# Kernel optimization log

Hardware: AMD Instinct MI355X
Metric: run time of the kernel (lower is better)

## Reference

```python
import jax, jax.numpy as jnp
import numpy as np

L, H, NH, NKV, HD, S, P, FF = 2, 2048, 16, 2, 128, 1024, 1024, 5632
G = NH // NKV
THETA = 1000000.0
EPS = 1e-6
SCALE = 1.0 / np.sqrt(HD).astype(np.float32)


def rms_norm(x, w):
    return x * jax.lax.rsqrt(jnp.mean(x * x, axis=-1, keepdims=True) + EPS) * w


def rotate_half(x):
    x1, x2 = jnp.split(x, 2, axis=-1)
    return jnp.concatenate([-x2, x1], axis=-1)


def setup_inputs() -> dict:
    key = jax.random.key(0)
    ks = iter(jax.random.split(key, 16))
    w = lambda shape: jax.random.normal(next(ks), shape, jnp.float32) * 0.02
    return {
        'inputs_embeds': jax.random.normal(next(ks), (1, S, H), jnp.float32),
        'position_ids': (jnp.arange(S, dtype=jnp.int32) + P)[None, :],
        'past_k': jax.random.normal(next(ks), (L, 1, NKV, P, HD), jnp.float32),
        'past_v': jax.random.normal(next(ks), (L, 1, NKV, P, HD), jnp.float32),
        'ln1_w': jnp.ones((L, H), jnp.float32),
        'wq': w((L, H, NH * HD)), 'bq': jnp.zeros((L, NH * HD), jnp.float32),
        'wk': w((L, H, NKV * HD)), 'bk': jnp.zeros((L, NKV * HD), jnp.float32),
        'wv': w((L, H, NKV * HD)), 'bv': jnp.zeros((L, NKV * HD), jnp.float32),
        'wo': w((L, NH * HD, H)),
        'ln2_w': jnp.ones((L, H), jnp.float32),
        'w_gate': w((L, H, FF)), 'w_up': w((L, H, FF)), 'w_down': w((L, FF, H)),
        'norm_w': jnp.ones((H,), jnp.float32),
    }


def reference(inputs_embeds, position_ids, past_k, past_v, ln1_w, wq, bq, wk, bk,
              wv, bv, wo, ln2_w, w_gate, w_up, w_down, norm_w):
    pos = position_ids.astype(jnp.float32)                      # [1,S]
    inv_freq = 1.0 / (THETA ** (jnp.arange(0, HD, 2, dtype=jnp.float32) / HD))
    freqs = pos[:, :, None] * inv_freq                          # [1,S,HD/2]
    emb = jnp.concatenate([freqs, freqs], axis=-1)              # [1,S,HD]
    cos = jnp.cos(emb)[:, None]                                 # [1,1,S,HD]
    sin = jnp.sin(emb)[:, None]
    T = P + S
    k_pos = jnp.arange(T, dtype=jnp.float32)
    # causal mask over absolute positions: future keys masked with -65504
    mask = jnp.where(k_pos[None, None, None, :] > pos[:, None, :, None],
                     jnp.float32(-65504.0), jnp.float32(0.0))   # [1,1,S,T]

    hidden = inputs_embeds
    present = []
    for i in range(L):
        residual = hidden
        h = rms_norm(hidden, ln1_w[i])
        q = (h @ wq[i] + bq[i]).reshape(1, S, NH, HD).transpose(0, 2, 1, 3)
        k = (h @ wk[i] + bk[i]).reshape(1, S, NKV, HD).transpose(0, 2, 1, 3)
        v = (h @ wv[i] + bv[i]).reshape(1, S, NKV, HD).transpose(0, 2, 1, 3)
        q = q * cos + rotate_half(q) * sin
        k = k * cos + rotate_half(k) * sin
        k = jnp.concatenate([past_k[i], k], axis=2)             # [1,NKV,T,HD]
        v = jnp.concatenate([past_v[i], v], axis=2)
        present.append(k)
        present.append(v)
        # GQA: group query heads per kv head instead of expanding k/v
        qg = q.reshape(1, NKV, G, S, HD)
        attn = jnp.einsum('bkgsd,bktd->bkgst', qg, k) * SCALE   # [1,NKV,G,S,T]
        attn = jax.nn.softmax(attn + mask[:, :, None], axis=-1)
        out = jnp.einsum('bkgst,bktd->bkgsd', attn, v)
        out = out.reshape(1, NH, S, HD).transpose(0, 2, 1, 3).reshape(1, S, H)
        hidden = residual + out @ wo[i]
        residual = hidden
        h = rms_norm(hidden, ln2_w[i])
        h = (jax.nn.silu(h @ w_gate[i]) * (h @ w_up[i])) @ w_down[i]
        hidden = residual + h
    hidden = rms_norm(hidden, norm_w)
    return (hidden, *present)
```

## Files before the change

### kernel.cpp

```cpp
#include <hip/hip_runtime.h>

#define L_ 2
#define H_ 2048
#define NH_ 16
#define NKV_ 2
#define HD_ 128
#define S_ 1024
#define P_ 1024
#define T_ 2048
#define FF_ 5632
#define QKVN_ 2560
#define KOFF_ 2048
#define VOFF_ 2304

#define EPS_ 1e-6f
#define SCALE_ 0.08838834764831845f
#define DEFER_THR_ 8.0f

typedef __bf16 bf16_t;
typedef unsigned int u32;
typedef __bf16 bx8 __attribute__((ext_vector_type(8)));
typedef __bf16 bx4 __attribute__((ext_vector_type(4)));
typedef float  fx4 __attribute__((ext_vector_type(4)));

__device__ __forceinline__ fx4 mfma16(bx8 a, bx8 b, fx4 c) {
  return __builtin_amdgcn_mfma_f32_16x16x32_bf16(a, b, c, 0, 0, 0);
}

#define GLL16(gsrc, ldst) __builtin_amdgcn_global_load_lds( \
    (__attribute__((address_space(1))) void*)(gsrc),        \
    (__attribute__((address_space(3))) void*)(ldst), 16, 0, 0)

__device__ __forceinline__ bx8 lds_read_b128(char* p) {
  u32 a = (u32)(uintptr_t)(__attribute__((address_space(3))) void*)p;
  bx8 d;
  asm volatile("ds_read_b128 %0, %1" : "=v"(d) : "v"(a));
  return d;
}
__device__ __forceinline__ void lds_write_b16(char* p, float v) {
  u32 a = (u32)(uintptr_t)(__attribute__((address_space(3))) void*)p;
  bf16_t b = (bf16_t)v;
  u32 d = (u32)__builtin_bit_cast(unsigned short, b);
  asm volatile("ds_write_b16 %0, %1" :: "v"(a), "v"(d));
}

#define LGKM(n) asm volatile("s_waitcnt lgkmcnt(" #n ")" ::: "memory"); __builtin_amdgcn_sched_barrier(0)

__device__ __forceinline__ int xcd_swizzle(int orig, int nwg) {
  int q = nwg >> 3, r = nwg & 7;
  int xcd = orig & 7, lid = orig >> 3;
  return (xcd < r ? xcd * (q + 1) : r * (q + 1) + (xcd - r) * q) + lid;
}

__global__ void k_rope_tables(const int* __restrict__ pos, float* __restrict__ ct, float* __restrict__ st) {
  int i = blockIdx.x * 256 + threadIdx.x;
  if (i >= S_ * 64) return;
  int s = i >> 6, d = i & 63;
  float p = (float)pos[s];
  float inv = expf(-(float)(2 * d) * (13.815510557964274f / 128.0f));
  float f = p * inv;
  ct[i] = cosf(f);
  st[i] = sinf(f);
}

__global__ void k_copy4(const float* __restrict__ in, float* __restrict__ out, int n4) {
  int i = blockIdx.x * 256 + threadIdx.x;
  if (i < n4) ((fx4*)out)[i] = ((const fx4*)in)[i];
}

__global__ void k_cbias(const float* __restrict__ bq, const float* __restrict__ bk,
                        const float* __restrict__ bv, float* __restrict__ cb) {
  int i = blockIdx.x * 256 + threadIdx.x;
  if (i >= L_ * QKVN_) return;
  int l = i / QKVN_, j = i % QKVN_;
  float v;
  if (j < KOFF_)      v = bq[l * KOFF_ + j];
  else if (j < VOFF_) v = bk[l * (NKV_ * HD_) + j - KOFF_];
  else                v = bv[l * (NKV_ * HD_) + j - VOFF_];
  cb[i] = v;
}

template<int OUTBF>
__global__ __launch_bounds__(256) void k_rmsnorm(const float* __restrict__ x, const float* __restrict__ w,
                                                 void* __restrict__ y) {
  int row = blockIdx.x, tid = threadIdx.x;
  const fx4* xr = (const fx4*)(x + (size_t)row * H_);
  fx4 v0 = xr[tid], v1 = xr[tid + 256];
  float ss = v0[0]*v0[0] + v0[1]*v0[1] + v0[2]*v0[2] + v0[3]*v0[3]
           + v1[0]*v1[0] + v1[1]*v1[1] + v1[2]*v1[2] + v1[3]*v1[3];
  #pragma unroll
  for (int off = 32; off > 0; off >>= 1) ss += __shfl_xor(ss, off);
  __shared__ float red[4];
  if ((tid & 63) == 0) red[tid >> 6] = ss;
  __syncthreads();
  float tot = red[0] + red[1] + red[2] + red[3];
  float rs = rsqrtf(tot * (1.0f / H_) + EPS_);
  const fx4* wr_ = (const fx4*)w;
  fx4 w0 = wr_[tid], w1 = wr_[tid + 256];
  if (OUTBF) {
    bf16_t* yb = (bf16_t*)y + (size_t)row * H_;
    bx4 o0, o1;
    #pragma unroll
    for (int i = 0; i < 4; i++) { o0[i] = (bf16_t)(v0[i] * rs * w0[i]); o1[i] = (bf16_t)(v1[i] * rs * w1[i]); }
    *(bx4*)&yb[tid * 4] = o0;
    *(bx4*)&yb[(tid + 256) * 4] = o1;
  } else {
    float* yf = (float*)y + (size_t)row * H_;
    fx4 o0, o1;
    #pragma unroll
    for (int i = 0; i < 4; i++) { o0[i] = v0[i] * rs * w0[i]; o1[i] = v1[i] * rs * w1[i]; }
    *(fx4*)&yf[tid * 4] = o0;
    *(fx4*)&yf[(tid + 256) * 4] = o1;
  }
}

__global__ __launch_bounds__(256) void k_transpose_w(const float* __restrict__ in, bf16_t* __restrict__ out,
                                                     int R, int C) {
  __shared__ __attribute__((aligned(16))) float Tt[64 * 68];
  int tid = threadIdx.x;
  int c0 = blockIdx.x * 64, r0 = blockIdx.y * 64;
  #pragma unroll
  for (int j = 0; j < 4; j++) {
    int c = j * 256 + tid;
    int row = c >> 4, col = (c & 15) * 4;
    *(fx4*)&Tt[row * 68 + col] = *(const fx4*)&in[(size_t)(r0 + row) * C + c0 + col];
  }
  __syncthreads();
  #pragma unroll
  for (int j = 0; j < 2; j++) {
    int c = j * 256 + tid;
    int n = c >> 3, ko = (c & 7) * 8;
    bx8 o;
    #pragma unroll
    for (int i = 0; i < 8; i++) o[i] = (bf16_t)Tt[(ko + i) * 68 + n];
    *(bx8*)&out[(size_t)(c0 + n) * R + r0 + ko] = o;
  }
}

template<int OUTBF, int HASB, int HASR, int HASG>
__global__ __launch_bounds__(256) void k_gemm(const bf16_t* __restrict__ A, const bf16_t* __restrict__ Bt,
                                              const float* __restrict__ bias, const float* __restrict__ res,
                                              const bf16_t* __restrict__ gmul,
                                              void* __restrict__ out, int M, int N, int K, int gy) {
  __shared__ __attribute__((aligned(16))) bf16_t sA[3][64 * 64];
  __shared__ __attribute__((aligned(16))) bf16_t sB[3][128 * 64];
  int tid = threadIdx.x;
  int w = tid >> 6, lane = tid & 63, g = lane >> 4, r = lane & 15;
  int wr = w >> 1, wc = w & 1;
  int swzid = xcd_swizzle((int)blockIdx.x, (int)gridDim.x);
  int m0 = (swzid % gy) * 64;
  int n0 = (swzid / gy) * 128;
  fx4 acc[2][4] = {};
  int swz = (r & 7) << 4;
  int col0 = (g * 16) ^ swz;
  int col1 = (64 + g * 16) ^ swz;
  int wbase = (tid & ~63) * 16;
  int nk = K >> 6;

  auto STAGE = [&](int buf, int k0) {
    #pragma unroll
    for (int j = 0; j < 2; j++) {
      int d = (j * 256 + tid) * 16;
      int row = d >> 7;
      int inrow = (d & 127) ^ ((row & 7) << 4);
      GLL16((const char*)(A + (size_t)(m0 + row) * K + k0) + inrow,
            (char*)&sA[buf][0] + j * 4096 + wbase);
    }
    #pragma unroll
    for (int j = 0; j < 4; j++) {
      int d = (j * 256 + tid) * 16;
      int row = d >> 7;
      int inrow = (d & 127) ^ ((row & 7) << 4);
      GLL16((const char*)(Bt + (size_t)(n0 + row) * K + k0) + inrow,
            (char*)&sB[buf][0] + j * 4096 + wbase);
    }
  };

  STAGE(0, 0);
  STAGE(1, 64);
  asm volatile("s_waitcnt vmcnt(6)" ::: "memory");
  __builtin_amdgcn_s_barrier();
  __builtin_amdgcn_sched_barrier(0);
  int cur = 0;
  for (int t = 0; t < nk; t++) {
    if (t + 2 < nk) STAGE((cur + 2) % 3, (t + 2) << 6);
    char* pa = (char*)&sA[cur][0] + (wr * 32 + r) * 128;
    char* pb = (char*)&sB[cur][0] + (wc * 64 + r) * 128;
    bx8 fa[2][2], fb[4][2];
    #pragma unroll
    for (int m = 0; m < 2; m++) {
      fa[m][0] = lds_read_b128(pa + m * 2048 + col0);
      fa[m][1] = lds_read_b128(pa + m * 2048 + col1);
    }
    #pragma unroll
    for (int n = 0; n < 4; n++) {
      fb[n][0] = lds_read_b128(pb + n * 2048 + col0);
      fb[n][1] = lds_read_b128(pb + n * 2048 + col1);
    }
    LGKM(0);
    #pragma unroll
    for (int kk = 0; kk < 2; kk++)
      #pragma unroll
      for (int n = 0; n < 4; n++) {
        acc[0][n] = mfma16(fa[0][kk], fb[n][kk], acc[0][n]);
        acc[1][n] = mfma16(fa[1][kk], fb[n][kk], acc[1][n]);
      }
    if (t + 1 < nk) {
      if (t + 2 < nk) { asm volatile("s_waitcnt vmcnt(6)" ::: "memory"); }
      else            { asm volatile("s_waitcnt vmcnt(0)" ::: "memory"); }
      __builtin_amdgcn_s_barrier();
      __builtin_amdgcn_sched_barrier(0);
    }
    cur = (cur + 1) % 3;
  }
  #pragma unroll
  for (int m = 0; m < 2; m++)
    #pragma unroll
    for (int n = 0; n < 4; n++) {
      int col = n0 + wc * 64 + n * 16 + r;
      #pragma unroll
      for (int rr = 0; rr < 4; rr++) {
        int row = m0 + wr * 32 + m * 16 + 4 * g + rr;
        float v = acc[m][n][rr];
        if (HASB) v += bias[col];
        if (HASR) v += res[(size_t)row * N + col];
        if (HASG) {
          float x = (float)gmul[(size_t)row * N + col];
          v = (x / (1.0f + __expf(-x))) * v;
        }
        if (OUTBF) ((bf16_t*)out)[(size_t)row * N + col] = (bf16_t)v;
        else       ((float*)out)[(size_t)row * N + col] = v;
      }
    }
}

__global__ void k_rope_q(const bf16_t* __restrict__ qkv, const float* __restrict__ ct,
                         const float* __restrict__ st, bf16_t* __restrict__ qout) {
  int i = blockIdx.x * 256 + threadIdx.x;
  if (i >= S_ * NH_ * 64) return;
  int d = i & 63, h = (i >> 6) & 15, s = i >> 10;
  size_t ib = (size_t)s * QKVN_ + h * HD_;
  float x1 = (float)qkv[ib + d];
  float x2 = (float)qkv[ib + d + 64];
  float c = ct[s * 64 + d], sn = st[s * 64 + d];
  size_t ob = ((size_t)h * S_ + s) * HD_;
  qout[ob + d]      = (bf16_t)(x1 * c - x2 * sn);
  qout[ob + d + 64] = (bf16_t)(x2 * c + x1 * sn);
}

__global__ void k_build_k(const bf16_t* __restrict__ qkv, const float* __restrict__ pastk,
                          const float* __restrict__ ct, const float* __restrict__ st,
                          bf16_t* __restrict__ kc, float* __restrict__ pk_out) {
  int i = blockIdx.x * 256 + threadIdx.x;
  if (i >= NKV_ * T_ * 64) return;
  int d = i & 63, t = (i >> 6) & (T_ - 1), kv = i >> 17;
  size_t cb = ((size_t)kv * T_ + t) * HD_;
  if (t < P_) {
    size_t pb = ((size_t)kv * P_ + t) * HD_;
    float a = pastk[pb + d], b = pastk[pb + d + 64];
    kc[cb + d] = (bf16_t)a; kc[cb + d + 64] = (bf16_t)b;
    pk_out[cb + d] = a;     pk_out[cb + d + 64] = b;
  } else {
    int s = t - P_;
    size_t ib = (size_t)s * QKVN_ + KOFF_ + kv * HD_;
    float x1 = (float)qkv[ib + d];
    float x2 = (float)qkv[ib + d + 64];
    float c = ct[s * 64 + d], sn = st[s * 64 + d];
    float k1 = x1 * c - x2 * sn, k2 = x2 * c + x1 * sn;
    kc[cb + d] = (bf16_t)k1; kc[cb + d + 64] = (bf16_t)k2;
    pk_out[cb + d] = k1;     pk_out[cb + d + 64] = k2;
  }
}

__global__ __launch_bounds__(256) void k_build_vt(const bf16_t* __restrict__ qkv, const float* __restrict__ pastv,
                                                  bf16_t* __restrict__ vt, float* __restrict__ pv_out) {
  int t0 = blockIdx.x * 64, d0 = blockIdx.y * 64, kv = blockIdx.z;
  __shared__ __attribute__((aligned(16))) float Tt[64 * 68];
  int tid = threadIdx.x;
  if (t0 < P_) {
    #pragma unroll
    for (int j = 0; j < 4; j++) {
      int c = j * 256 + tid;
      int row = c >> 4, col = (c & 15) * 4;
      int t = t0 + row;
      fx4 v = *(const fx4*)&pastv[((size_t)kv * P_ + t) * HD_ + d0 + col];
      *(fx4*)&Tt[row * 68 + col] = v;
      *(fx4*)&pv_out[((size_t)kv * T_ + t) * HD_ + d0 + col] = v;
    }
  } else {
    #pragma unroll
    for (int j = 0; j < 4; j++) {
      int c = j * 256 + tid;
      int row = c >> 4, col = (c & 15) * 4;
      int t = t0 + row;
      bx4 b = *(const bx4*)&qkv[(size_t)(t - P_) * QKVN_ + VOFF_ + kv * HD_ + d0 + col];
      fx4 v;
      #pragma unroll
      for (int q = 0; q < 4; q++) v[q] = (float)b[q];
      *(fx4*)&Tt[row * 68 + col] = v;
      *(fx4*)&pv_out[((size_t)kv * T_ + t) * HD_ + d0 + col] = v;
    }
  }
  __syncthreads();
  #pragma unroll
  for (int j = 0; j < 2; j++) {
    int c = j * 256 + tid;
    int n = c >> 3, ko = (c & 7) * 8;
    bx8 o;
    #pragma unroll
    for (int i = 0; i < 8; i++) o[i] = (bf16_t)Tt[(ko + i) * 68 + n];
    *(bx8*)&vt[((size_t)kv * HD_ + d0 + n) * T_ + t0 + ko] = o;
  }
}

__global__ __launch_bounds__(128) void k_attn(const bf16_t* __restrict__ Q, const bf16_t* __restrict__ Kc,
                                              const bf16_t* __restrict__ VT, bf16_t* __restrict__ O) {
  __shared__ __attribute__((aligned(16))) bf16_t Klds[2][64 * 128];
  __shared__ __attribute__((aligned(16))) bf16_t Vlds[2][128 * 64];
  __shared__ __attribute__((aligned(16))) bf16_t Plds[2][16][72];
  int tid = threadIdx.x;
  int w = tid >> 6, lane = tid & 63, g = lane >> 4, r = lane & 15;
  int h = blockIdx.y, kv = h >> 3;
  int m0 = blockIdx.x * 32;
  int qr0 = m0 + w * 16;
  const bf16_t* qb = Q + ((size_t)h * S_ + qr0 + r) * HD_ + g * 8;
  bx8 qf[4];
  #pragma unroll
  for (int kc = 0; kc < 4; kc++) qf[kc] = *(const bx8*)(qb + kc * 32);
  fx4 of[8] = {};
  float mrun[4], lrun[4];
  #pragma unroll
  for (int i = 0; i < 4; i++) { mrun[i] = -1e30f; lrun[i] = 0.0f; }
  int lim = P_ + qr0 + 4 * g;
  int ntile = (P_ + m0 + 32 + 63) >> 6;
  const char* kg = (const char*)(Kc + (size_t)kv * T_ * HD_);
  const char* vg = (const char*)(VT + (size_t)kv * HD_ * T_);
  int wbase = (tid & ~63) * 16;

  auto STAGE = [&](int buf, int t0) {
    #pragma unroll
    for (int j = 0; j < 8; j++) {
      int D = j * 2048 + tid * 16;
      int row = D >> 8, inrow = D & 255;
      const char* src = kg + (size_t)(t0 + row) * 256 + (inrow ^ ((row & 7) << 4));
      GLL16(src, (char*)&Klds[buf][0] + j * 2048 + wbase);
    }
    #pragma unroll
    for (int j = 0; j < 8; j++) {
      int D = j * 2048 + tid * 16;
      int row = D >> 7, inrow = D & 127;
      const char* src = vg + (size_t)row * 4096 + (size_t)t0 * 2 + (inrow ^ ((row & 7) << 4));
      GLL16(src, (char*)&Vlds[buf][0] + j * 2048 + wbase);
    }
  };

  STAGE(0, 0);
  asm volatile("s_waitcnt vmcnt(0)" ::: "memory");
  __builtin_amdgcn_s_barrier();
  __builtin_amdgcn_sched_barrier(0);
  int cur = 0;
  for (int t = 0; t < ntile; t++) {
    int t0 = t * 64;
    if (t + 1 < ntile) {
      STAGE(cur ^ 1, t0 + 64);
      asm volatile("s_waitcnt vmcnt(16)" ::: "memory");
    } else {
      asm volatile("s_waitcnt vmcnt(0)" ::: "memory");
    }
    __builtin_amdgcn_s_barrier();
    __builtin_amdgcn_sched_barrier(0);
    char* kb = (char*)&Klds[cur][0];
    bx8 kf[4][4];
    #pragma unroll
    for (int nt = 0; nt < 4; nt++) {
      int row = nt * 16 + r;
      char* kr = kb + row * 256;
      int sz = (row & 7) << 4;
      #pragma unroll
      for (int kc = 0; kc < 4; kc++)
        kf[nt][kc] = lds_read_b128(kr + (((kc * 32 + g * 8) * 2) ^ sz));
    }
    fx4 sc[4] = {};
    LGKM(12);
    #pragma unroll
    for (int kc = 0; kc < 4; kc++) sc[0] = mfma16(qf[kc], kf[0][kc], sc[0]);
    LGKM(8);
    #pragma unroll
    for (int kc = 0; kc < 4; kc++) sc[1] = mfma16(qf[kc], kf[1][kc], sc[1]);
    LGKM(4);
    #pragma unroll
    for (int kc = 0; kc < 4; kc++) sc[2] = mfma16(qf[kc], kf[2][kc], sc[2]);
    LGKM(0);
    #pragma unroll
    for (int kc = 0; kc < 4; kc++) sc[3] = mfma16(qf[kc], kf[3][kc], sc[3]);
    float lm[4] = {-1e30f, -1e30f, -1e30f, -1e30f};
    #pragma unroll
    for (int nt = 0; nt < 4; nt++)
      #pragma unroll
      for (int rr = 0; rr < 4; rr++) {
        int key = t0 + nt * 16 + r;
        float sv = sc[nt][rr] * SCALE_;
        sv = (key > lim + rr) ? -1e30f : sv;
        sc[nt][rr] = sv;
        lm[rr] = fmaxf(lm[rr], sv);
      }
    int ok = (lm[0] <= mrun[0] + DEFER_THR_) & (lm[1] <= mrun[1] + DEFER_THR_) &
             (lm[2] <= mrun[2] + DEFER_THR_) & (lm[3] <= mrun[3] + DEFER_THR_);
    if (!__all(ok)) {
      float av[4];
      #pragma unroll
      for (int off = 1; off < 16; off <<= 1)
        #pragma unroll
        for (int rr = 0; rr < 4; rr++) lm[rr] = fmaxf(lm[rr], __shfl_xor(lm[rr], off));
      #pragma unroll
      for (int rr = 0; rr < 4; rr++) {
        float mn = fmaxf(mrun[rr], lm[rr]);
        av[rr] = __expf(mrun[rr] - mn);
        mrun[rr] = mn;
        lrun[rr] *= av[rr];
      }
      #pragma unroll
      for (int f = 0; f < 8; f++)
        #pragma unroll
        for (int rr = 0; rr < 4; rr++) of[f][rr] *= av[rr];
    }
    #pragma unroll
    for (int nt = 0; nt < 4; nt++)
      #pragma unroll
      for (int rr = 0; rr < 4; rr++) {
        float pr = __expf(sc[nt][rr] - mrun[rr]);
        lrun[rr] += pr;
        lds_write_b16((char*)&Plds[w][4 * g + rr][nt * 16 + r], pr);
      }
    LGKM(0);
    char* vb = (char*)&Vlds[cur][0];
    bx8 pa0 = lds_read_b128((char*)&Plds[w][r][g * 8]);
    bx8 vf0[8], vf1[8];
    #pragma unroll
    for (int dt = 0; dt < 8; dt++) {
      int row = dt * 16 + r;
      vf0[dt] = lds_read_b128(vb + row * 128 + (((g * 8) * 2) ^ ((row & 7) << 4)));
    }
    bx8 pa1 = lds_read_b128((char*)&Plds[w][r][32 + g * 8]);
    #pragma unroll
    for (int dt = 0; dt < 8; dt++) {
      int row = dt * 16 + r;
      vf1[dt] = lds_read_b128(vb + row * 128 + (((32 + g * 8) * 2) ^ ((row & 7) << 4)));
    }
    LGKM(9);
    #pragma unroll
    for (int dt = 0; dt < 8; dt++) of[dt] = mfma16(pa0, vf0[dt], of[dt]);
    LGKM(0);
    #pragma unroll
    for (int dt = 0; dt < 8; dt++) of[dt] = mfma16(pa1, vf1[dt], of[dt]);
    __builtin_amdgcn_s_barrier();
    cur ^= 1;
  }
  #pragma unroll
  for (int off = 1; off < 16; off <<= 1)
    #pragma unroll
    for (int rr = 0; rr < 4; rr++) lrun[rr] += __shfl_xor(lrun[rr], off);
  float li[4];
  #pragma unroll
  for (int rr = 0; rr < 4; rr++) li[rr] = 1.0f / lrun[rr];
  #pragma unroll
  for (int dt = 0; dt < 8; dt++)
    #pragma unroll
    for (int rr = 0; rr < 4; rr++)
      O[(size_t)(qr0 + 4 * g + rr) * H_ + h * HD_ + dt * 16 + r] = (bf16_t)(of[dt][rr] * li[rr]);
}

extern "C" void kernel_launch(void* const* d_in, const int* in_sizes, int n_in,
                              void* d_out, int out_size, void* d_ws, size_t ws_size,
                              hipStream_t stream) {
  const float* embeds = (const float*)d_in[0];
  const int*   pos    = (const int*)d_in[1];
  const float* past_k = (const float*)d_in[2];
  const float* past_v = (const float*)d_in[3];
  const float* ln1    = (const float*)d_in[4];
  const float* wq     = (const float*)d_in[5];
  const float* bq     = (const float*)d_in[6];
  const float* wk     = (const float*)d_in[7];
  const float* bk     = (const float*)d_in[8];
  const float* wv     = (const float*)d_in[9];
  const float* bv     = (const float*)d_in[10];
  const float* wo     = (const float*)d_in[11];
  const float* ln2    = (const float*)d_in[12];
  const float* wg     = (const float*)d_in[13];
  const float* wu     = (const float*)d_in[14];
  const float* wd     = (const float*)d_in[15];
  const float* normw  = (const float*)d_in[16];

  char* wsp = (char*)d_ws;
  auto take = [&](size_t n) { char* p = wsp; wsp += (n + 255) & ~(size_t)255; return (void*)p; };
  float*  cos_t  = (float*)take((size_t)S_ * 64 * 4);
  float*  sin_t  = (float*)take((size_t)S_ * 64 * 4);
  float*  cbias  = (float*)take((size_t)L_ * QKVN_ * 4);
  float*  hidden = (float*)take((size_t)S_ * H_ * 4);
  bf16_t* hnorm  = (bf16_t*)take((size_t)S_ * H_ * 2);
  bf16_t* qkv    = (bf16_t*)take((size_t)S_ * QKVN_ * 2);
  bf16_t* qrope  = (bf16_t*)take((size_t)NH_ * S_ * HD_ * 2);
  bf16_t* kcache = (bf16_t*)take((size_t)NKV_ * T_ * HD_ * 2);
  bf16_t* vtr    = (bf16_t*)take((size_t)NKV_ * HD_ * T_ * 2);
  bf16_t* attno  = (bf16_t*)take((size_t)S_ * H_ * 2);
  bf16_t* gateb  = (bf16_t*)take((size_t)S_ * FF_ * 2);
  bf16_t* hgb    = (bf16_t*)take((size_t)S_ * FF_ * 2);
  bf16_t* wT     = (bf16_t*)take((size_t)FF_ * H_ * 2);

  float* out_h = (float*)d_out;

  k_rope_tables<<<256, 256, 0, stream>>>(pos, cos_t, sin_t);
  k_cbias<<<(L_ * QKVN_ + 255) / 256, 256, 0, stream>>>(bq, bk, bv, cbias);
  k_copy4<<<(S_ * H_ / 4 + 255) / 256, 256, 0, stream>>>(embeds, hidden, S_ * H_ / 4);

  for (int l = 0; l < L_; l++) {
    const float* wq_l = wq + (size_t)l * H_ * (NH_ * HD_);
    const float* wk_l = wk + (size_t)l * H_ * (NKV_ * HD_);
    const float* wv_l = wv + (size_t)l * H_ * (NKV_ * HD_);
    const float* wo_l = wo + (size_t)l * (NH_ * HD_) * H_;
    const float* wg_l = wg + (size_t)l * H_ * FF_;
    const float* wu_l = wu + (size_t)l * H_ * FF_;
    const float* wd_l = wd + (size_t)l * FF_ * H_;
    const float* pk_in = past_k + (size_t)l * NKV_ * P_ * HD_;
    const float* pv_in = past_v + (size_t)l * NKV_ * P_ * HD_;
    float* pk_out = out_h + (size_t)S_ * H_ + (size_t)l * 2 * NKV_ * T_ * HD_;
    float* pv_out = pk_out + (size_t)NKV_ * T_ * HD_;

    k_rmsnorm<1><<<S_, 256, 0, stream>>>(hidden, ln1 + (size_t)l * H_, hnorm);
    k_transpose_w<<<dim3(32, 32), 256, 0, stream>>>(wq_l, wT, H_, NH_ * HD_);
    k_transpose_w<<<dim3(4, 32), 256, 0, stream>>>(wk_l, wT + (size_t)KOFF_ * H_, H_, NKV_ * HD_);
    k_transpose_w<<<dim3(4, 32), 256, 0, stream>>>(wv_l, wT + (size_t)VOFF_ * H_, H_, NKV_ * HD_);
    k_gemm<1, 1, 0, 0><<<(QKVN_ / 128) * (S_ / 64), 256, 0, stream>>>(
        hnorm, wT, cbias + (size_t)l * QKVN_, nullptr, nullptr, qkv, S_, QKVN_, H_, S_ / 64);
    k_rope_q<<<(S_ * NH_ * 64) / 256, 256, 0, stream>>>(qkv, cos_t, sin_t, qrope);
    k_build_k<<<(NKV_ * T_ * 64) / 256, 256, 0, stream>>>(qkv, pk_in, cos_t, sin_t, kcache, pk_out);
    k_build_vt<<<dim3(T_ / 64, HD_ / 64, NKV_), 256, 0, stream>>>(qkv, pv_in, vtr, pv_out);
    k_attn<<<dim3(S_ / 32, NH_), 128, 0, stream>>>(qrope, kcache, vtr, attno);
    k_transpose_w<<<dim3(32, 32), 256, 0, stream>>>(wo_l, wT, NH_ * HD_, H_);
    k_gemm<0, 0, 1, 0><<<(H_ / 128) * (S_ / 64), 256, 0, stream>>>(
        attno, wT, nullptr, hidden, nullptr, hidden, S_, H_, NH_ * HD_, S_ / 64);
    k_rmsnorm<1><<<S_, 256, 0, stream>>>(hidden, ln2 + (size_t)l * H_, hnorm);
    k_transpose_w<<<dim3(88, 32), 256, 0, stream>>>(wg_l, wT, H_, FF_);
    k_gemm<1, 0, 0, 0><<<(FF_ / 128) * (S_ / 64), 256, 0, stream>>>(
        hnorm, wT, nullptr, nullptr, nullptr, gateb, S_, FF_, H_, S_ / 64);
    k_transpose_w<<<dim3(88, 32), 256, 0, stream>>>(wu_l, wT, H_, FF_);
    k_gemm<1, 0, 0, 1><<<(FF_ / 128) * (S_ / 64), 256, 0, stream>>>(
        hnorm, wT, nullptr, nullptr, gateb, hgb, S_, FF_, H_, S_ / 64);
    k_transpose_w<<<dim3(32, 88), 256, 0, stream>>>(wd_l, wT, FF_, H_);
    k_gemm<0, 0, 1, 0><<<(H_ / 128) * (S_ / 64), 256, 0, stream>>>(
        hgb, wT, nullptr, hidden, nullptr, hidden, S_, H_, FF_, S_ / 64);
  }
  k_rmsnorm<0><<<S_, 256, 0, stream>>>(hidden, normw, out_h);
}
```

Before: 586.0 us.

## Process two 16-row query subtiles per wave in attention to reuse K/V fragments

Each wave in the attention kernel now handles 32 query rows as two 16-row subtiles, so the block covers 64 query rows and the grid halves. Every K and V fragment read from LDS feeds two MFMAs instead of one, which cuts LDS traffic and global K/V staging per query row. The cost is about double the accumulator and softmax-state registers, which may lower occupancy. It also launches fewer blocks, so load balance across the causal tiles gets coarser.

```diff
diff --git a/kernel.cpp b/kernel.cpp
--- a/kernel.cpp
+++ b/kernel.cpp
@@ -317,22 +317,28 @@
                                               const bf16_t* __restrict__ VT, bf16_t* __restrict__ O) {
   __shared__ __attribute__((aligned(16))) bf16_t Klds[2][64 * 128];
   __shared__ __attribute__((aligned(16))) bf16_t Vlds[2][128 * 64];
-  __shared__ __attribute__((aligned(16))) bf16_t Plds[2][16][72];
+  __shared__ __attribute__((aligned(16))) bf16_t Plds[2][2][16][72];
   int tid = threadIdx.x;
   int w = tid >> 6, lane = tid & 63, g = lane >> 4, r = lane & 15;
   int h = blockIdx.y, kv = h >> 3;
-  int m0 = blockIdx.x * 32;
-  int qr0 = m0 + w * 16;
-  const bf16_t* qb = Q + ((size_t)h * S_ + qr0 + r) * HD_ + g * 8;
-  bx8 qf[4];
-  #pragma unroll
-  for (int kc = 0; kc < 4; kc++) qf[kc] = *(const bx8*)(qb + kc * 32);
-  fx4 of[8] = {};
-  float mrun[4], lrun[4];
-  #pragma unroll
-  for (int i = 0; i < 4; i++) { mrun[i] = -1e30f; lrun[i] = 0.0f; }
-  int lim = P_ + qr0 + 4 * g;
-  int ntile = (P_ + m0 + 32 + 63) >> 6;
+  int m0 = blockIdx.x * 64;
+  int qr0 = m0 + w * 32;
+  bx8 qf[2][4];
+  #pragma unroll
+  for (int qs = 0; qs < 2; qs++) {
+    const bf16_t* qb = Q + ((size_t)h * S_ + qr0 + qs * 16 + r) * HD_ + g * 8;
+    #pragma unroll
+    for (int kc = 0; kc < 4; kc++) qf[qs][kc] = *(const bx8*)(qb + kc * 32);
+  }
+  fx4 of[2][8] = {};
+  float mrun[2][4], lrun[2][4];
+  #pragma unroll
+  for (int qs = 0; qs < 2; qs++)
+    #pragma unroll
+    for (int i = 0; i < 4; i++) { mrun[qs][i] = -1e30f; lrun[qs][i] = 0.0f; }
+  int lim0 = P_ + qr0 + 4 * g;
+  int lim1 = lim0 + 16;
+  int ntile = (P_ + m0 + 64) >> 6;
   const char* kg = (const char*)(Kc + (size_t)kv * T_ * HD_);
   const char* vg = (const char*)(VT + (size_t)kv * HD_ * T_);
   int wbase = (tid & ~63) * 16;
@@ -370,104 +376,135 @@
     __builtin_amdgcn_s_barrier();
     __builtin_amdgcn_sched_barrier(0);
     char* kb = (char*)&Klds[cur][0];
-    bx8 kf[4][4];
-    #pragma unroll
-    for (int nt = 0; nt < 4; nt++) {
+    auto krd = [&](int nt, int kc) -> bx8 {
       int row = nt * 16 + r;
-      char* kr = kb + row * 256;
-      int sz = (row & 7) << 4;
-      #pragma unroll
-      for (int kc = 0; kc < 4; kc++)
-        kf[nt][kc] = lds_read_b128(kr + (((kc * 32 + g * 8) * 2) ^ sz));
-    }
-    fx4 sc[4] = {};
-    LGKM(12);
-    #pragma unroll
-    for (int kc = 0; kc < 4; kc++) sc[0] = mfma16(qf[kc], kf[0][kc], sc[0]);
-    LGKM(8);
-    #pragma unroll
-    for (int kc = 0; kc < 4; kc++) sc[1] = mfma16(qf[kc], kf[1][kc], sc[1]);
+      return lds_read_b128(kb + row * 256 + (((kc * 32 + g * 8) * 2) ^ ((row & 7) << 4)));
+    };
+    fx4 sc[2][4] = {};
+    bx8 kfA[4], kfB[4];
+    #pragma unroll
+    for (int kc = 0; kc < 4; kc++) kfA[kc] = krd(0, kc);
+    #pragma unroll
+    for (int kc = 0; kc < 4; kc++) kfB[kc] = krd(1, kc);
     LGKM(4);
     #pragma unroll
-    for (int kc = 0; kc < 4; kc++) sc[2] = mfma16(qf[kc], kf[2][kc], sc[2]);
+    for (int kc = 0; kc < 4; kc++) {
+      sc[0][0] = mfma16(qf[0][kc], kfA[kc], sc[0][0]);
+      sc[1][0] = mfma16(qf[1][kc], kfA[kc], sc[1][0]);
+    }
+    #pragma unroll
+    for (int kc = 0; kc < 4; kc++) kfA[kc] = krd(2, kc);
+    LGKM(4);
+    #pragma unroll
+    for (int kc = 0; kc < 4; kc++) {
+      sc[0][1] = mfma16(qf[0][kc], kfB[kc], sc[0][1]);
+      sc[1][1] = mfma16(qf[1][kc], kfB[kc], sc[1][1]);
+    }
+    #pragma unroll
+    for (int kc = 0; kc < 4; kc++) kfB[kc] = krd(3, kc);
+    LGKM(4);
+    #pragma unroll
+    for (int kc = 0; kc < 4; kc++) {
+      sc[0][2] = mfma16(qf[0][kc], kfA[kc], sc[0][2]);
+      sc[1][2] = mfma16(qf[1][kc], kfA[kc], sc[1][2]);
+    }
     LGKM(0);
     #pragma unroll
-    for (int kc = 0; kc < 4; kc++) sc[3] = mfma16(qf[kc], kf[3][kc], sc[3]);
-    float lm[4] = {-1e30f, -1e30f, -1e30f, -1e30f};
-    #pragma unroll
-    for (int nt = 0; nt < 4; nt++)
-      #pragma unroll
-      for (int rr = 0; rr < 4; rr++) {
-        int key = t0 + nt * 16 + r;
-        float sv = sc[nt][rr] * SCALE_;
-        sv = (key > lim + rr) ? -1e30f : sv;
-        sc[nt][rr] = sv;
-        lm[rr] = fmaxf(lm[rr], sv);
+    for (int kc = 0; kc < 4; kc++) {
+      sc[0][3] = mfma16(qf[0][kc], kfB[kc], sc[0][3]);
+      sc[1][3] = mfma16(qf[1][kc], kfB[kc], sc[1][3]);
+    }
+    float lm[2][4];
+    #pragma unroll
+    for (int qs = 0; qs < 2; qs++) {
+      int lim = qs ? lim1 : lim0;
+      #pragma unroll
+      for (int rr = 0; rr < 4; rr++) lm[qs][rr] = -1e30f;
+      #pragma unroll
+      for (int nt = 0; nt < 4; nt++)
+        #pragma unroll
+        for (int rr = 0; rr < 4; rr++) {
+          int key = t0 + nt * 16 + r;
+          float sv = sc[qs][nt][rr] * SCALE_;
+          sv = (key > lim + rr) ? -1e30f : sv;
+          sc[qs][nt][rr] = sv;
+          lm[qs][rr] = fmaxf(lm[qs][rr], sv);
+        }
+    }
+    int ok = 1;
+    #pragma unroll
+    for (int qs = 0; qs < 2; qs++)
+      #pragma unroll
+      for (int rr = 0; rr < 4; rr++) ok &= (lm[qs][rr] <= mrun[qs][rr] + DEFER_THR_);
+    if (!__all(ok)) {
+      #pragma unroll
+      for (int qs = 0; qs < 2; qs++) {
+        float av[4];
+        #pragma unroll
+        for (int off = 1; off < 16; off <<= 1)
+          #pragma unroll
+          for (int rr = 0; rr < 4; rr++) lm[qs][rr] = fmaxf(lm[qs][rr], __shfl_xor(lm[qs][rr], off));
+        #pragma unroll
+        for (int rr = 0; rr < 4; rr++) {
+          float mn = fmaxf(mrun[qs][rr], lm[qs][rr]);
+          av[rr] = __expf(mrun[qs][rr] - mn);
+          mrun[qs][rr] = mn;
+          lrun[qs][rr] *= av[rr];
+        }
+        #pragma unroll
+        for (int f = 0; f < 8; f++)
+          #pragma unroll
+          for (int rr = 0; rr < 4; rr++) of[qs][f][rr] *= av[rr];
       }
-    int ok = (lm[0] <= mrun[0] + DEFER_THR_) & (lm[1] <= mrun[1] + DEFER_THR_) &
-             (lm[2] <= mrun[2] + DEFER_THR_) & (lm[3] <= mrun[3] + DEFER_THR_);
-    if (!__all(ok)) {
-      float av[4];
-      #pragma unroll
-      for (int off = 1; off < 16; off <<= 1)
+    }
+    #pragma unroll
+    for (int qs = 0; qs < 2; qs++)
+      #pragma unroll
+      for (int nt = 0; nt < 4; nt++)
         #pragma unroll
-        for (int rr = 0; rr < 4; rr++) lm[rr] = fmaxf(lm[rr], __shfl_xor(lm[rr], off));
-      #pragma unroll
-      for (int rr = 0; rr < 4; rr++) {
-        float mn = fmaxf(mrun[rr], lm[rr]);
-        av[rr] = __expf(mrun[rr] - mn);
-        mrun[rr] = mn;
-        lrun[rr] *= av[rr];
-      }
-      #pragma unroll
-      for (int f = 0; f < 8; f++)
-        #pragma unroll
-        for (int rr = 0; rr < 4; rr++) of[f][rr] *= av[rr];
-    }
-    #pragma unroll
-    for (int nt = 0; nt < 4; nt++)
-      #pragma unroll
-      for (int rr = 0; rr < 4; rr++) {
-        float pr = __expf(sc[nt][rr] - mrun[rr]);
-        lrun[rr] += pr;
-        lds_write_b16((char*)&Plds[w][4 * g + rr][nt * 16 + r], pr);
-      }
+        for (int rr = 0; rr < 4; rr++) {
+          float pr = __expf(sc[qs][nt][rr] - mrun[qs][rr]);
+          lrun[qs][rr] += pr;
+          lds_write_b16((char*)&Plds[w][qs][4 * g + rr][nt * 16 + r], pr);
+        }
     LGKM(0);
     char* vb = (char*)&Vlds[cur][0];
-    bx8 pa0 = lds_read_b128((char*)&Plds[w][r][g * 8]);
-    bx8 vf0[8], vf1[8];
-    #pragma unroll
-    for (int dt = 0; dt < 8; dt++) {
-      int row = dt * 16 + r;
-      vf0[dt] = lds_read_b128(vb + row * 128 + (((g * 8) * 2) ^ ((row & 7) << 4)));
-    }
-    bx8 pa1 = lds_read_b128((char*)&Plds[w][r][32 + g * 8]);
-    #pragma unroll
-    for (int dt = 0; dt < 8; dt++) {
-      int row = dt * 16 + r;
-      vf1[dt] = lds_read_b128(vb + row * 128 + (((32 + g * 8) * 2) ^ ((row & 7) << 4)));
-    }
-    LGKM(9);
-    #pragma unroll
-    for (int dt = 0; dt < 8; dt++) of[dt] = mfma16(pa0, vf0[dt], of[dt]);
-    LGKM(0);
-    #pragma unroll
-    for (int dt = 0; dt < 8; dt++) of[dt] = mfma16(pa1, vf1[dt], of[dt]);
+    #pragma unroll
+    for (int ks = 0; ks < 2; ks++) {
+      bx8 pa0 = lds_read_b128((char*)&Plds[w][0][r][ks * 32 + g * 8]);
+      bx8 pa1 = lds_read_b128((char*)&Plds[w][1][r][ks * 32 + g * 8]);
+      bx8 vf[8];
+      #pragma unroll
+      for (int dt = 0; dt < 8; dt++) {
+        int row = dt * 16 + r;
+        vf[dt] = lds_read_b128(vb + row * 128 + (((ks * 32 + g * 8) * 2) ^ ((row & 7) << 4)));
+      }
+      LGKM(0);
+      #pragma unroll
+      for (int dt = 0; dt < 8; dt++) {
+        of[0][dt] = mfma16(pa0, vf[dt], of[0][dt]);
+        of[1][dt] = mfma16(pa1, vf[dt], of[1][dt]);
+      }
+    }
     __builtin_amdgcn_s_barrier();
     cur ^= 1;
   }
   #pragma unroll
-  for (int off = 1; off < 16; off <<= 1)
-    #pragma unroll
-    for (int rr = 0; rr < 4; rr++) lrun[rr] += __shfl_xor(lrun[rr], off);
-  float li[4];
-  #pragma unroll
-  for (int rr = 0; rr < 4; rr++) li[rr] = 1.0f / lrun[rr];
-  #pragma unroll
-  for (int dt = 0; dt < 8; dt++)
-    #pragma unroll
-    for (int rr = 0; rr < 4; rr++)
-      O[(size_t)(qr0 + 4 * g + rr) * H_ + h * HD_ + dt * 16 + r] = (bf16_t)(of[dt][rr] * li[rr]);
+  for (int qs = 0; qs < 2; qs++) {
+    #pragma unroll
+    for (int off = 1; off < 16; off <<= 1)
+      #pragma unroll
+      for (int rr = 0; rr < 4; rr++) lrun[qs][rr] += __shfl_xor(lrun[qs][rr], off);
+    float li[4];
+    #pragma unroll
+    for (int rr = 0; rr < 4; rr++) li[rr] = 1.0f / lrun[qs][rr];
+    #pragma unroll
+    for (int dt = 0; dt < 8; dt++)
+      #pragma unroll
+      for (int rr = 0; rr < 4; rr++)
+        O[(size_t)(qr0 + qs * 16 + 4 * g + rr) * H_ + h * HD_ + dt * 16 + r] =
+            (bf16_t)(of[qs][dt][rr] * li[rr]);
+  }
 }
 
 extern "C" void kernel_launch(void* const* d_in, const int* in_sizes, int n_in,
@@ -535,7 +572,7 @@
     k_rope_q<<<(S_ * NH_ * 64) / 256, 256, 0, stream>>>(qkv, cos_t, sin_t, qrope);
     k_build_k<<<(NKV_ * T_ * 64) / 256, 256, 0, stream>>>(qkv, pk_in, cos_t, sin_t, kcache, pk_out);
     k_build_vt<<<dim3(T_ / 64, HD_ / 64, NKV_), 256, 0, stream>>>(qkv, pv_in, vtr, pv_out);
-    k_attn<<<dim3(S_ / 32, NH_), 128, 0, stream>>>(qrope, kcache, vtr, attno);
+    k_attn<<<dim3(S_ / 64, NH_), 128, 0, stream>>>(qrope, kcache, vtr, attno);
     k_transpose_w<<<dim3(32, 32), 256, 0, stream>>>(wo_l, wT, NH_ * HD_, H_);
     k_gemm<0, 0, 1, 0><<<(H_ / 128) * (S_ / 64), 256, 0, stream>>>(
         attno, wT, nullptr, hidden, nullptr, hidden, S_, H_, NH_ * HD_, S_ / 64);
```

Result: slower. 620.6 us (+5.9%).
